# Optimization experiments

Measured on AMD Instinct MI355X. Metric: run time of the kernel, lower is better.

The kernel has to match this reference:

```python
import jax, jax.numpy as jnp
import numpy as np

B, IN, H = 4096, 1024, 1024


def setup_inputs() -> dict:
    key = jax.random.key(0)
    ks = jax.random.split(key, 20)
    s_in = 1.0 / np.sqrt(IN)
    s_h = 1.0 / np.sqrt(H)
    def lin(kw, kb, fan_in, scale):
        W = jax.random.uniform(kw, (H, fan_in), jnp.float32, -scale, scale)
        b = jax.random.uniform(kb, (H,), jnp.float32, -scale, scale)
        return W, b
    Wxf, bxf = lin(ks[0], ks[1], IN, s_in)
    Whf, bhf = lin(ks[2], ks[3], H, s_h)
    Wxi, bxi = lin(ks[4], ks[5], IN, s_in)
    Whi, bhi = lin(ks[6], ks[7], H, s_h)
    Wxo, bxo = lin(ks[8], ks[9], IN, s_in)
    Who, bho = lin(ks[10], ks[11], H, s_h)
    Wxc, bxc = lin(ks[12], ks[13], IN, s_in)
    Whc, bhc = lin(ks[14], ks[15], H, s_h)
    x = jax.random.normal(ks[16], (B, IN), jnp.float32)
    c = jax.random.normal(ks[17], (B, H), jnp.float32)
    h = jax.random.normal(ks[18], (B, H), jnp.float32)
    return dict(x=x, c=c, h=h,
                Wxf=Wxf, bxf=bxf, Whf=Whf, bhf=bhf,
                Wxi=Wxi, bxi=bxi, Whi=Whi, bhi=bhi,
                Wxo=Wxo, bxo=bxo, Who=Who, bho=bho,
                Wxc=Wxc, bxc=bxc, Whc=Whc, bhc=bhc)


def reference(x, c, h,
              Wxf, bxf, Whf, bhf,
              Wxi, bxi, Whi, bhi,
              Wxo, bxo, Who, bho,
              Wxc, bxc, Whc, bhc):
    # Fuse the 8 small GEMMs into two batched GEMMs: x @ Wx^T and h @ Wh^T
    # with gate outputs concatenated along the hidden dim [f, i, o, c~].
    Wx = jnp.concatenate([Wxf, Wxi, Wxo, Wxc], axis=0)   # [4H, IN]
    Wh = jnp.concatenate([Whf, Whi, Who, Whc], axis=0)   # [4H, H]
    bx = jnp.concatenate([bxf, bxi, bxo, bxc], axis=0)   # [4H]
    bh = jnp.concatenate([bhf, bhi, bho, bhc], axis=0)   # [4H]
    gates = x @ Wx.T + h @ Wh.T + (bx + bh)              # [B, 4H]
    hs = Wxf.shape[0]
    f = jax.nn.sigmoid(gates[:, 0 * hs:1 * hs])
    i = jax.nn.sigmoid(gates[:, 1 * hs:2 * hs])
    o = jax.nn.sigmoid(gates[:, 2 * hs:3 * hs])
    ctil = jnp.tanh(gates[:, 3 * hs:4 * hs])
    ct = f * c + ctil * i
    ht = jnp.tanh(ct) * o
    return (ct, ht)
```

## Files before the change

kernel.cpp:

```cpp
#include <hip/hip_runtime.h>
#include <hip/hip_bf16.h>
#include <stdint.h>

typedef __hip_bfloat16 bf16;
typedef __attribute__((ext_vector_type(8))) short short8;
typedef __attribute__((ext_vector_type(4))) float floatx4;

#define AS1(p) ((const __attribute__((address_space(1))) void*)(p))
#define AS3(p) ((__attribute__((address_space(3))) void*)(p))

#define M_DIM 4096
#define H_DIM 1024
#define MEG   (1u << 20)
#define LDS_BUF 24576

__device__ __forceinline__ unsigned short f2bf(float f) {
    uint32_t u = __float_as_uint(f);
    uint32_t r = (u + 0x7FFFu + ((u >> 16) & 1u)) >> 16;
    return (unsigned short)r;
}

__device__ __forceinline__ float fast_sigmoid(float v) {
    return 1.0f / (1.0f + __expf(-v));
}
__device__ __forceinline__ float fast_tanh(float v) {
    return 2.0f / (1.0f + __expf(-2.0f * v)) - 1.0f;
}

__global__ __launch_bounds__(256)
void pack_bf16(const float* __restrict__ x, const float* __restrict__ h,
               const float* Wxf, const float* Wxi, const float* Wxo, const float* Wxc,
               const float* Whf, const float* Whi, const float* Who, const float* Whc,
               unsigned short* __restrict__ ws)
{
    const int w = threadIdx.x >> 6;
    const int l = threadIdx.x & 63;
    const uint32_t W = blockIdx.x * 4u + (uint32_t)w;

    const uint32_t r  = (uint32_t)l >> 2;
    const uint32_t kg = ((uint32_t)l & 3u) ^ ((r >> 1) & 3u);

    const float* src;
    uint32_t row, kt;
    if (W < 16384u) {
        const uint32_t Wa = W & 8191u;
        const uint32_t ch = Wa & 7u;
        kt = (Wa >> 3) & 31u;
        const uint32_t mx = Wa >> 8;
        src = (W < 8192u) ? x : h;
        row = mx * 128u + ch * 16u + r;
    } else {
        const uint32_t V = W & 8191u;
        kt = V & 31u;
        uint32_t U = V >> 5;
        const uint32_t b4 = U & 3u;
        const uint32_t g  = (U >> 2) & 3u;
        const uint32_t ny = U >> 4;
        if (W < 24576u)
            src = (g == 0) ? Wxf : (g == 1) ? Wxi : (g == 2) ? Wxo : Wxc;
        else
            src = (g == 0) ? Whf : (g == 1) ? Whi : (g == 2) ? Who : Whc;
        row = ny * 64u + b4 * 16u + r;
    }
    const float* s = src + (size_t)row * 1024u + kt * 32u + kg * 8u;
    const float4 v0 = *(const float4*)s;
    const float4 v1 = *(const float4*)(s + 4);
    short8 pk;
    pk[0] = (short)f2bf(v0.x); pk[1] = (short)f2bf(v0.y);
    pk[2] = (short)f2bf(v0.z); pk[3] = (short)f2bf(v0.w);
    pk[4] = (short)f2bf(v1.x); pk[5] = (short)f2bf(v1.y);
    pk[6] = (short)f2bf(v1.z); pk[7] = (short)f2bf(v1.w);
    *(short8*)(ws + (size_t)W * 512u + (uint32_t)l * 8u) = pk;
}

__global__ __launch_bounds__(512, 4)
void lstm_fused_kernel(const unsigned short* __restrict__ ws,
                       const float* __restrict__ c,
                       const float* __restrict__ bxf, const float* __restrict__ bhf,
                       const float* __restrict__ bxi, const float* __restrict__ bhi,
                       const float* __restrict__ bxo, const float* __restrict__ bho,
                       const float* __restrict__ bxc, const float* __restrict__ bhc,
                       float* __restrict__ out)
{
    __shared__ __align__(16) char lds[3 * LDS_BUF];

    const int tid  = threadIdx.x;
    const int w    = tid >> 6;
    const int lane = tid & 63;

    const int bid = blockIdx.x;
    const int mx  = bid >> 4;
    const int ny  = ((bid & 7) << 1) | ((bid >> 3) & 1);
    const int bm0 = mx * 128;
    const int bn0 = ny * 64;

    const unsigned short* srcP0[3];
    const unsigned short* srcP1[3];
    uint32_t kstr[3];
    uint32_t loff[3];
#pragma unroll
    for (int i = 0; i < 3; ++i) {
        const int ch = w * 3 + i;
        if (ch < 8) {
            const uint32_t base = ((uint32_t)mx * 32u * 8u + (uint32_t)ch) * 512u;
            srcP0[i] = ws + base + (uint32_t)lane * 8u;
            srcP1[i] = srcP0[i] + (8u << 20);
            kstr[i]  = 8u * 512u;
            loff[i]  = (uint32_t)ch * 1024u;
        } else {
            const int b  = ch - 8;
            const uint32_t g  = (uint32_t)b >> 2;
            const uint32_t b4 = (uint32_t)b & 3u;
            const uint32_t base = (16384u + ((uint32_t)ny * 16u + g * 4u + b4) * 32u) * 512u;
            srcP0[i] = ws + base + (uint32_t)lane * 8u;
            srcP1[i] = srcP0[i] + (8192u * 512u);
            kstr[i]  = 512u;
            loff[i]  = 8192u + (uint32_t)b * 1024u;
        }
    }
#pragma unroll
    for (int i = 0; i < 3; ++i) {
        const int ch = w * 3 + i;
        if (ch < 8) srcP1[i] = srcP0[i] + 8192u * 512u;
    }

    const int wrow  = (w & 1) * 64;
    const int wcol  = (w >> 1) * 16;
    const int lrc   = lane & 15;
    const int lquad = lane >> 4;

    const uint32_t kslot = (((uint32_t)lquad ^ (((uint32_t)lrc >> 1) & 3u))) * 8u;

    uint32_t aoff[4];
#pragma unroll
    for (int mt = 0; mt < 4; ++mt)
        aoff[mt] = (uint32_t)((wrow + mt * 16 + lrc) * 32) + kslot;
    uint32_t boff[4];
#pragma unroll
    for (int g = 0; g < 4; ++g)
        boff[g] = (uint32_t)(g * 2048 + (wcol + lrc) * 32) + kslot;

    floatx4 acc[4][4];
#pragma unroll
    for (int g = 0; g < 4; ++g)
#pragma unroll
        for (int mt = 0; mt < 4; ++mt)
            acc[g][mt] = (floatx4){0.f, 0.f, 0.f, 0.f};

    auto issue_loads = [&](int kt, uint32_t stage) {
        const int phase = kt >> 5;
        const uint32_t kk = (uint32_t)(kt & 31);
        const uint32_t bb = stage * LDS_BUF;
#pragma unroll
        for (int i = 0; i < 3; ++i) {
            const unsigned short* src = (phase ? srcP1[i] : srcP0[i]) + kk * kstr[i];
            __builtin_amdgcn_global_load_lds(AS1(src), AS3(lds + bb + loff[i]), 16, 0, 0);
        }
    };
    auto compute = [&](uint32_t stage) {
        const char* base = lds + stage * LDS_BUF;
        const bf16* lA = (const bf16*)base;
        const bf16* lB = (const bf16*)(base + 8192);
        short8 afr[4];
#pragma unroll
        for (int mt = 0; mt < 4; ++mt)
            afr[mt] = *(const short8*)(lA + aoff[mt]);
#pragma unroll
        for (int g = 0; g < 4; ++g) {
            const short8 bfr = *(const short8*)(lB + boff[g]);
#pragma unroll
            for (int mt = 0; mt < 4; ++mt)
                acc[g][mt] = __builtin_amdgcn_mfma_f32_16x16x32_bf16(
                    afr[mt], bfr, acc[g][mt], 0, 0, 0);
        }
    };

    issue_loads(0, 0);
    issue_loads(1, 1);

    uint32_t s_comp = 0;
    uint32_t s_load = 2;
    for (int kt = 0; kt < 62; ++kt) {
        asm volatile("s_waitcnt vmcnt(3)\ns_barrier" ::: "memory");
        issue_loads(kt + 2, s_load);
        compute(s_comp);
        s_comp = (s_comp == 2) ? 0 : s_comp + 1;
        s_load = (s_load == 2) ? 0 : s_load + 1;
    }
    asm volatile("s_waitcnt vmcnt(3)\ns_barrier" ::: "memory");
    compute(s_comp);
    s_comp = (s_comp == 2) ? 0 : s_comp + 1;
    asm volatile("s_waitcnt vmcnt(0)\ns_barrier" ::: "memory");
    compute(s_comp);

    float* out_ct = out;
    float* out_ht = out + (size_t)M_DIM * H_DIM;
    {
        const int col = bn0 + wcol + lrc;
        const float bf_ = bxf[col] + bhf[col];
        const float bi_ = bxi[col] + bhi[col];
        const float bo_ = bxo[col] + bho[col];
        const float bc_ = bxc[col] + bhc[col];
#pragma unroll
        for (int mt = 0; mt < 4; ++mt) {
#pragma unroll
            for (int r = 0; r < 4; ++r) {
                const int row = bm0 + wrow + mt * 16 + lquad * 4 + r;
                const float gf = acc[0][mt][r] + bf_;
                const float gi = acc[1][mt][r] + bi_;
                const float go = acc[2][mt][r] + bo_;
                const float gc = acc[3][mt][r] + bc_;
                const float f    = fast_sigmoid(gf);
                const float ii   = fast_sigmoid(gi);
                const float o    = fast_sigmoid(go);
                const float ctil = fast_tanh(gc);
                const float cv   = c[(size_t)row * H_DIM + col];
                const float ctn  = f * cv + ctil * ii;
                const float htn  = fast_tanh(ctn) * o;
                out_ct[(size_t)row * H_DIM + col] = ctn;
                out_ht[(size_t)row * H_DIM + col] = htn;
            }
        }
    }
}

extern "C" void kernel_launch(void* const* d_in, const int* in_sizes, int n_in,
                              void* d_out, int out_size, void* d_ws, size_t ws_size,
                              hipStream_t stream) {
    (void)in_sizes; (void)n_in; (void)out_size; (void)ws_size;
    const float* x   = (const float*)d_in[0];
    const float* c   = (const float*)d_in[1];
    const float* h   = (const float*)d_in[2];
    const float* Wxf = (const float*)d_in[3];  const float* bxf = (const float*)d_in[4];
    const float* Whf = (const float*)d_in[5];  const float* bhf = (const float*)d_in[6];
    const float* Wxi = (const float*)d_in[7];  const float* bxi = (const float*)d_in[8];
    const float* Whi = (const float*)d_in[9];  const float* bhi = (const float*)d_in[10];
    const float* Wxo = (const float*)d_in[11]; const float* bxo = (const float*)d_in[12];
    const float* Who = (const float*)d_in[13]; const float* bho = (const float*)d_in[14];
    const float* Wxc = (const float*)d_in[15]; const float* bxc = (const float*)d_in[16];
    const float* Whc = (const float*)d_in[17]; const float* bhc = (const float*)d_in[18];
    float* out = (float*)d_out;
    unsigned short* ws = (unsigned short*)d_ws;

    pack_bf16<<<8192, 256, 0, stream>>>(x, h,
        Wxf, Wxi, Wxo, Wxc, Whf, Whi, Who, Whc, ws);

    lstm_fused_kernel<<<512, 512, 0, stream>>>(ws, c,
        bxf, bhf, bxi, bhi, bxo, bho, bxc, bhc, out);
}
```

Before: 207.1 us.

## Stage global tiles through registers into double-buffered LDS

Replaces the direct global-to-LDS loads (global_load_lds) over a three-stage LDS ring with ordinary global loads into registers, which are then written to a two-stage LDS double buffer one half-iteration later. The main loop is unrolled by two, and each barrier now waits on lgkmcnt instead of vmcnt. The aim is to shrink LDS per block so more blocks fit per CU, and to give the compiler explicit control over load latency. In exchange it costs extra VGPRs for the staged chunks and extra VALU/LDS write instructions. Each global load also gets only one compute step to hide its latency before the compiler-inserted vmcnt wait.

```diff
diff --git a/kernel.cpp b/kernel.cpp
--- a/kernel.cpp
+++ b/kernel.cpp
@@ -6,13 +6,10 @@
 typedef __attribute__((ext_vector_type(8))) short short8;
 typedef __attribute__((ext_vector_type(4))) float floatx4;
 
-#define AS1(p) ((const __attribute__((address_space(1))) void*)(p))
-#define AS3(p) ((__attribute__((address_space(3))) void*)(p))
-
 #define M_DIM 4096
 #define H_DIM 1024
-#define MEG   (1u << 20)
 #define LDS_BUF 24576
+#define PHOFF 4194304u
 
 __device__ __forceinline__ unsigned short f2bf(float f) {
     uint32_t u = __float_as_uint(f);
@@ -82,7 +79,7 @@
                        const float* __restrict__ bxc, const float* __restrict__ bhc,
                        float* __restrict__ out)
 {
-    __shared__ __align__(16) char lds[3 * LDS_BUF];
+    __shared__ __align__(16) char lds[2 * LDS_BUF];
 
     const int tid  = threadIdx.x;
     const int w    = tid >> 6;
@@ -94,34 +91,26 @@
     const int bm0 = mx * 128;
     const int bn0 = ny * 64;
 
-    const unsigned short* srcP0[3];
-    const unsigned short* srcP1[3];
+    const unsigned short* srcP[3];
     uint32_t kstr[3];
-    uint32_t loff[3];
+    uint32_t loffL[3];
 #pragma unroll
     for (int i = 0; i < 3; ++i) {
         const int ch = w * 3 + i;
         if (ch < 8) {
-            const uint32_t base = ((uint32_t)mx * 32u * 8u + (uint32_t)ch) * 512u;
-            srcP0[i] = ws + base + (uint32_t)lane * 8u;
-            srcP1[i] = srcP0[i] + (8u << 20);
-            kstr[i]  = 8u * 512u;
-            loff[i]  = (uint32_t)ch * 1024u;
+            const uint32_t base = ((uint32_t)mx * 256u + (uint32_t)ch) * 512u;
+            srcP[i] = ws + base + (uint32_t)lane * 8u;
+            kstr[i] = 8u * 512u;
+            loffL[i] = (uint32_t)ch * 1024u + (uint32_t)lane * 16u;
         } else {
             const int b  = ch - 8;
             const uint32_t g  = (uint32_t)b >> 2;
             const uint32_t b4 = (uint32_t)b & 3u;
             const uint32_t base = (16384u + ((uint32_t)ny * 16u + g * 4u + b4) * 32u) * 512u;
-            srcP0[i] = ws + base + (uint32_t)lane * 8u;
-            srcP1[i] = srcP0[i] + (8192u * 512u);
-            kstr[i]  = 512u;
-            loff[i]  = 8192u + (uint32_t)b * 1024u;
+            srcP[i] = ws + base + (uint32_t)lane * 8u;
+            kstr[i] = 512u;
+            loffL[i] = 8192u + (uint32_t)b * 1024u + (uint32_t)lane * 16u;
         }
-    }
-#pragma unroll
-    for (int i = 0; i < 3; ++i) {
-        const int ch = w * 3 + i;
-        if (ch < 8) srcP1[i] = srcP0[i] + 8192u * 512u;
     }
 
     const int wrow  = (w & 1) * 64;
@@ -147,15 +136,20 @@
         for (int mt = 0; mt < 4; ++mt)
             acc[g][mt] = (floatx4){0.f, 0.f, 0.f, 0.f};
 
-    auto issue_loads = [&](int kt, uint32_t stage) {
-        const int phase = kt >> 5;
-        const uint32_t kk = (uint32_t)(kt & 31);
-        const uint32_t bb = stage * LDS_BUF;
-#pragma unroll
-        for (int i = 0; i < 3; ++i) {
-            const unsigned short* src = (phase ? srcP1[i] : srcP0[i]) + kk * kstr[i];
-            __builtin_amdgcn_global_load_lds(AS1(src), AS3(lds + bb + loff[i]), 16, 0, 0);
-        }
+    short8 R0[3], R1[3];
+
+    auto load_chunks = [&](int kl, short8 (&R)[3]) {
+        const uint32_t off = ((kl >= 32) ? PHOFF : 0u);
+        const uint32_t kk = (uint32_t)(kl & 31);
+#pragma unroll
+        for (int i = 0; i < 3; ++i)
+            R[i] = *(const short8*)(srcP[i] + off + kk * kstr[i]);
+    };
+    auto write_chunks = [&](short8 (&R)[3], uint32_t stage) {
+        char* base = lds + stage * LDS_BUF;
+#pragma unroll
+        for (int i = 0; i < 3; ++i)
+            *(short8*)(base + loffL[i]) = R[i];
     };
     auto compute = [&](uint32_t stage) {
         const char* base = lds + stage * LDS_BUF;
@@ -175,23 +169,25 @@
         }
     };
 
-    issue_loads(0, 0);
-    issue_loads(1, 1);
-
-    uint32_t s_comp = 0;
-    uint32_t s_load = 2;
-    for (int kt = 0; kt < 62; ++kt) {
-        asm volatile("s_waitcnt vmcnt(3)\ns_barrier" ::: "memory");
-        issue_loads(kt + 2, s_load);
-        compute(s_comp);
-        s_comp = (s_comp == 2) ? 0 : s_comp + 1;
-        s_load = (s_load == 2) ? 0 : s_load + 1;
-    }
-    asm volatile("s_waitcnt vmcnt(3)\ns_barrier" ::: "memory");
-    compute(s_comp);
-    s_comp = (s_comp == 2) ? 0 : s_comp + 1;
-    asm volatile("s_waitcnt vmcnt(0)\ns_barrier" ::: "memory");
-    compute(s_comp);
+    load_chunks(0, R0);
+    load_chunks(1, R1);
+    write_chunks(R0, 0);
+
+    for (int kt = 0; kt < 62; kt += 2) {
+        asm volatile("s_waitcnt lgkmcnt(0)\ns_barrier" ::: "memory");
+        load_chunks(kt + 2, R0);
+        write_chunks(R1, 1);
+        compute(0);
+        asm volatile("s_waitcnt lgkmcnt(0)\ns_barrier" ::: "memory");
+        load_chunks(kt + 3, R1);
+        write_chunks(R0, 0);
+        compute(1);
+    }
+    asm volatile("s_waitcnt lgkmcnt(0)\ns_barrier" ::: "memory");
+    write_chunks(R1, 1);
+    compute(0);
+    asm volatile("s_waitcnt lgkmcnt(0)\ns_barrier" ::: "memory");
+    compute(1);
 
     float* out_ct = out;
     float* out_ht = out + (size_t)M_DIM * H_DIM;
```

After: 217.1 us. 1.05x slower.
